# Optimization experiments

Hardware: AMD Instinct MI355X
Metric: run time of the kernel (lower is better)

## Reference

```python
import jax, jax.numpy as jnp
import numpy as np

N_NODES = 100000
IN_CH = 65
HID_CH = 64
N_EDGES = 3200000


def setup_inputs() -> dict:
    key = jax.random.key(0)
    k1, k2, k3, k4, k5 = jax.random.split(key, 5)
    x = jax.random.normal(k1, (N_NODES, IN_CH), dtype=jnp.float32)
    edge_index = jax.random.randint(k2, (2, N_EDGES), 0, N_NODES, dtype=jnp.int64)
    edge_weight = jax.random.uniform(k3, (N_EDGES,), dtype=jnp.float32)
    # PyG GraphConv params: lin_rel (with bias) applied to aggregated neighbors,
    # lin_root (no bias) applied to self features.
    scale = 1.0 / np.sqrt(IN_CH)
    W_rel = jax.random.uniform(k4, (HID_CH, IN_CH), dtype=jnp.float32, minval=-scale, maxval=scale)
    b_rel = jnp.zeros((HID_CH,), dtype=jnp.float32)
    W_root = jax.random.uniform(k5, (HID_CH, IN_CH), dtype=jnp.float32, minval=-scale, maxval=scale)
    return {"x": x, "edge_index": edge_index, "edge_weight": edge_weight,
            "W_rel": W_rel, "b_rel": b_rel, "W_root": W_root}


def reference(x, edge_index, edge_weight, W_rel, b_rel, W_root):
    src = edge_index[0]  # source nodes (x_j in PyG message)
    dst = edge_index[1]  # target nodes (aggregation index)
    # gather neighbor features, weight by edge weight: [E, IN_CH]
    msgs = x[src] * edge_weight[:, None]
    # scatter-add to destination nodes: [N, IN_CH]
    aggr = jax.ops.segment_sum(msgs, dst, num_segments=N_NODES)
    # out = lin_rel(aggr) + lin_root(x)
    out = aggr @ W_rel.T + b_rel + x @ W_root.T
    return out
```

## Files before the change

### kernel.cpp

```cpp
#include <hip/hip_runtime.h>

#define IN_CH 65
#define HID 64
#define BN 64
#define NB 1563
#define CAP 2560
#define SCAP 2432
#define EPB 16384
#define TPS 1024
#define EPT (EPB / TPS)
#define WSTR 132

static inline size_t align16(size_t v) { return (v + 15) & ~(size_t)15; }

__device__ inline ushort f2bf(float f) {
    uint u = __float_as_uint(f);
    return (ushort)((u + 0x7FFF + ((u >> 16) & 1)) >> 16);
}

__global__ __launch_bounds__(256) void k1y(const float* __restrict__ x,
                                           const float* __restrict__ W_rel,
                                           ushort* __restrict__ y16,
                                           int* __restrict__ cnt, int nBuckets,
                                           int nNodes) {
    __shared__ float xsT[65 * 132];
    __shared__ float ws[65 * 68];
    const int tid = threadIdx.x;
    const int tx = tid & 7;
    const int ty = tid >> 3;
    const long nodeBase = (long)blockIdx.x * 128;
    const int nValid = (int)min((long)128, (long)nNodes - nodeBase);

    if (cnt) {
        const int c2 = blockIdx.x * 2;
        if (tid == 0 && c2 < nBuckets) cnt[c2] = 0;
        if (tid == 1 && c2 + 1 < nBuckets) cnt[c2 + 1] = 0;
    }

    for (int f = tid; f < HID * IN_CH; f += 256) {
        const int j = f / IN_CH, c = f - j * IN_CH;
        ws[c * 68 + j] = W_rel[f];
    }
    const float* xsrc = x + nodeBase * IN_CH;
    for (int f = tid; f < 128 * IN_CH; f += 256) {
        const int node = f / IN_CH, k = f - node * IN_CH;
        xsT[k * 132 + node] = (node < nValid) ? xsrc[f] : 0.f;
    }
    __syncthreads();

    float acc[4][8];
#pragma unroll
    for (int i = 0; i < 4; ++i)
#pragma unroll
        for (int j = 0; j < 8; ++j) acc[i][j] = 0.f;

    const int r0 = ty * 4;
    const int c0 = tx * 8;
    for (int k = 0; k < IN_CH; ++k) {
        const float4 a4 = *(const float4*)&xsT[k * 132 + r0];
        const float4 b0 = *(const float4*)&ws[k * 68 + c0];
        const float4 b1 = *(const float4*)&ws[k * 68 + c0 + 4];
        const float aa[4] = {a4.x, a4.y, a4.z, a4.w};
        const float bb[8] = {b0.x, b0.y, b0.z, b0.w, b1.x, b1.y, b1.z, b1.w};
#pragma unroll
        for (int i = 0; i < 4; ++i)
#pragma unroll
            for (int j = 0; j < 8; ++j) acc[i][j] += aa[i] * bb[j];
    }

#pragma unroll
    for (int i = 0; i < 4; ++i) {
        const long node = nodeBase + r0 + i;
        if (node >= nNodes) break;
        uint4 pk;
        pk.x = (uint)f2bf(acc[i][0]) | ((uint)f2bf(acc[i][1]) << 16);
        pk.y = (uint)f2bf(acc[i][2]) | ((uint)f2bf(acc[i][3]) << 16);
        pk.z = (uint)f2bf(acc[i][4]) | ((uint)f2bf(acc[i][5]) << 16);
        pk.w = (uint)f2bf(acc[i][6]) | ((uint)f2bf(acc[i][7]) << 16);
        *(uint4*)&y16[node * HID + c0] = pk;
    }
}

__global__ __launch_bounds__(TPS) void scatterB(const int* __restrict__ ei,
                                                const float* __restrict__ ew,
                                                int* __restrict__ cnt,
                                                int2* __restrict__ pairs, int E) {
    __shared__ int lhist[NB];
    __shared__ int lbase[NB];
    const int tid = threadIdx.x;
    const long e0 = (long)blockIdx.x * EPB;
    const int n = (int)min((long)EPB, (long)E - e0);

    for (int i = tid; i < NB; i += TPS) lhist[i] = 0;
    __syncthreads();

    int dstv[EPT], srcv[EPT];
    float wv[EPT];
#pragma unroll
    for (int k = 0; k < EPT; ++k) {
        const int i = tid + k * TPS;
        const bool valid = i < n;
        dstv[k] = valid ? ei[(long)E + e0 + i] : 0;
        srcv[k] = valid ? ei[e0 + i] : 0;
        wv[k]   = valid ? ew[e0 + i] : 0.f;
        if (valid) atomicAdd(&lhist[dstv[k] >> 6], 1);
    }
    __syncthreads();

    for (int i = tid; i < NB; i += TPS) {
        const int c = lhist[i];
        lbase[i] = c ? atomicAdd(&cnt[i], c) : 0;
        lhist[i] = 0;
    }
    __syncthreads();

#pragma unroll
    for (int k = 0; k < EPT; ++k) {
        const int i = tid + k * TPS;
        if (i < n) {
            const int b = dstv[k] >> 6;
            const int p = lbase[b] + atomicAdd(&lhist[b], 1);
            if (p < CAP)
                pairs[(size_t)b * CAP + p] =
                    make_int2((srcv[k] << 7) | ((dstv[k] & (BN - 1)) << 25),
                              __float_as_int(wv[k]));
        }
    }
}

__global__ __launch_bounds__(512) void aggregateS16(const int2* __restrict__ pairs,
                                                    const int* __restrict__ cnt,
                                                    const ushort* __restrict__ y16,
                                                    const float* __restrict__ x,
                                                    const float* __restrict__ W_root,
                                                    const float* __restrict__ b_rel,
                                                    float* __restrict__ out, int N) {
    __shared__ __align__(16) char smem[19456 + 17408 + 4 * (BN + BN + 1 + BN) + 16];
    float* xs       = (float*)smem;
    int2*  sorted   = (int2*)smem;
    float* rootBuf  = (float*)(smem + 19456);
    int*   sH       = (int*)(smem + 36864);
    int*   soff     = sH + BN;
    int*   scur     = soff + BN + 1;

    const int tid = threadIdx.x;
    const int lane = tid & 63;
    const int wvid = tid >> 6;
    const int half = lane >> 5;
    const uint lane4 = (lane & 31) * 4;
    const int b = blockIdx.x;
    const long nodeBase = (long)b * BN;

    const int m = min(cnt[b], CAP);
    const int2* pb = pairs + (size_t)b * CAP;

    int2 pv[5];
#pragma unroll
    for (int kk = 0; kk < 5; ++kk) {
        const int i = tid + kk * 512;
        if (i < m) pv[kk] = pb[i];
    }

    const int nValid = (int)min((long)BN, (long)N - nodeBase);
    const int nx = nValid * IN_CH;
    const float* xsrc = x + nodeBase * IN_CH;
    for (int i = tid; i < BN * IN_CH; i += 512) xs[i] = (i < nx) ? xsrc[i] : 0.f;

    if (tid < BN) { sH[tid] = 0; scur[tid] = 0; }
    __syncthreads();

#pragma unroll
    for (int kk = 0; kk < 5; ++kk) {
        const int i = tid + kk * 512;
        if (i < m) atomicAdd(&sH[(uint)pv[kk].x >> 25], 1);
    }

    {
        const int wvu = __builtin_amdgcn_readfirstlane(wvid);
        const int c0 = wvu * 8;
        float racc[8];
#pragma unroll
        for (int j = 0; j < 8; ++j) racc[j] = b_rel[c0 + j];
        const float* xrow = xs + lane * IN_CH;
        const float* wb = W_root + (size_t)c0 * IN_CH;
        for (int k = 0; k < IN_CH; ++k) {
            const float xv = xrow[k];
#pragma unroll
            for (int j = 0; j < 8; ++j) racc[j] += xv * wb[j * IN_CH + k];
        }
        float* rb = rootBuf + lane * 68 + c0;
        *(float4*)(rb + 0) = make_float4(racc[0], racc[1], racc[2], racc[3]);
        *(float4*)(rb + 4) = make_float4(racc[4], racc[5], racc[6], racc[7]);
    }
    __syncthreads();

    for (int off = 1; off < BN; off <<= 1) {
        int v = 0;
        if (tid < BN) {
            v = sH[tid];
            if (tid >= off) v += sH[tid - off];
        }
        __syncthreads();
        if (tid < BN) sH[tid] = v;
        __syncthreads();
    }
    if (tid < BN) soff[tid + 1] = sH[tid];
    if (tid == 0) soff[0] = 0;
    __syncthreads();

#pragma unroll
    for (int kk = 0; kk < 5; ++kk) {
        const int i = tid + kk * 512;
        if (i < m) {
            const int d = (uint)pv[kk].x >> 25;
            const int slot = soff[d] + atomicAdd(&scur[d], 1);
            if (slot < SCAP) sorted[slot] = make_int2(pv[kk].x & 0x00FFFF80, pv[kk].y);
        }
    }
    __syncthreads();

    const char* yb = (const char*)y16;
    for (int nl = wvid; nl < BN; nl += 8) {
        const long node = nodeBase + nl;
        if (node >= N) break;
        const int kbeg = min(soff[nl], SCAP);
        const int kend = min(soff[nl + 1], SCAP);
        float ax = 0.f, ay = 0.f;
        int k = kbeg + half;
        for (; k + 14 < kend; k += 16) {
            int2 pp[8];
#pragma unroll
            for (int j = 0; j < 8; ++j) pp[j] = sorted[k + 2 * j];
            uint qq[8];
#pragma unroll
            for (int j = 0; j < 8; ++j)
                qq[j] = *(const uint*)(yb + (uint)pp[j].x + lane4);
#pragma unroll
            for (int j = 0; j < 8; ++j) {
                const float w = __int_as_float(pp[j].y);
                ax += w * __uint_as_float(qq[j] << 16);
                ay += w * __uint_as_float(qq[j] & 0xFFFF0000u);
            }
        }
        for (; k + 6 < kend; k += 8) {
            const int2 p0 = sorted[k],     p1 = sorted[k + 2];
            const int2 p2 = sorted[k + 4], p3 = sorted[k + 6];
            const uint q0 = *(const uint*)(yb + (uint)p0.x + lane4);
            const uint q1 = *(const uint*)(yb + (uint)p1.x + lane4);
            const uint q2 = *(const uint*)(yb + (uint)p2.x + lane4);
            const uint q3 = *(const uint*)(yb + (uint)p3.x + lane4);
            const float w0 = __int_as_float(p0.y), w1 = __int_as_float(p1.y);
            const float w2 = __int_as_float(p2.y), w3 = __int_as_float(p3.y);
            ax += w0 * __uint_as_float(q0 << 16);
            ay += w0 * __uint_as_float(q0 & 0xFFFF0000u);
            ax += w1 * __uint_as_float(q1 << 16);
            ay += w1 * __uint_as_float(q1 & 0xFFFF0000u);
            ax += w2 * __uint_as_float(q2 << 16);
            ay += w2 * __uint_as_float(q2 & 0xFFFF0000u);
            ax += w3 * __uint_as_float(q3 << 16);
            ay += w3 * __uint_as_float(q3 & 0xFFFF0000u);
        }
        for (; k < kend; k += 2) {
            const int2 p = sorted[k];
            const uint q = *(const uint*)(yb + (uint)p.x + lane4);
            const float w = __int_as_float(p.y);
            ax += w * __uint_as_float(q << 16);
            ay += w * __uint_as_float(q & 0xFFFF0000u);
        }
        ax += __shfl_xor(ax, 32);
        ay += __shfl_xor(ay, 32);
        if (half == 0) {
            const float2 rb = *(const float2*)&rootBuf[nl * 68 + (lane & 31) * 2];
            float2* o = (float2*)(out + node * HID) + (lane & 31);
            *o = make_float2(rb.x + ax, rb.y + ay);
        }
    }
}

__global__ __launch_bounds__(256) void k1_full(const float* __restrict__ x,
                                               const float* __restrict__ W_rel,
                                               const float* __restrict__ b_rel,
                                               const float* __restrict__ W_root,
                                               ushort* __restrict__ y16,
                                               float* __restrict__ out,
                                               int nNodes) {
    __shared__ float xs[64 * IN_CH];
    __shared__ float ws[IN_CH * WSTR];
    const int tid = threadIdx.x;
    const int tx = tid & 15;
    const int ty = tid >> 4;
    const long nodeBase = (long)blockIdx.x * 64;
    const int nValid = min(64, nNodes - (int)nodeBase);
    const int nx = nValid * IN_CH;

    for (int f = tid; f < HID * IN_CH; f += 256) {
        const int j = f / IN_CH, c = f - j * IN_CH;
        ws[c * WSTR + j] = W_rel[f];
    }
    for (int f = tid; f < HID * IN_CH; f += 256) {
        const int j = f / IN_CH, c = f - j * IN_CH;
        ws[c * WSTR + HID + j] = W_root[f];
    }
    const float* xsrc = x + nodeBase * IN_CH;
    for (int i = tid; i < 64 * IN_CH; i += 256) xs[i] = (i < nx) ? xsrc[i] : 0.f;
    __syncthreads();

    float acc[4][8];
#pragma unroll
    for (int i = 0; i < 4; ++i)
#pragma unroll
        for (int j = 0; j < 8; ++j) acc[i][j] = 0.f;

    const int r0 = ty * 4;
    const int c0 = tx * 8;
    for (int k = 0; k < IN_CH; ++k) {
        float aa[4] = {xs[(r0 + 0) * IN_CH + k], xs[(r0 + 1) * IN_CH + k],
                       xs[(r0 + 2) * IN_CH + k], xs[(r0 + 3) * IN_CH + k]};
        float4 b0 = *(const float4*)&ws[k * WSTR + c0];
        float4 b1 = *(const float4*)&ws[k * WSTR + c0 + 4];
        float bb[8] = {b0.x, b0.y, b0.z, b0.w, b1.x, b1.y, b1.z, b1.w};
#pragma unroll
        for (int i = 0; i < 4; ++i)
#pragma unroll
            for (int j = 0; j < 8; ++j) acc[i][j] += aa[i] * bb[j];
    }

    if (c0 >= HID) {
        const int h0 = c0 - HID;
        float4 bb0 = *(const float4*)&b_rel[h0];
        float4 bb1 = *(const float4*)&b_rel[h0 + 4];
        float bv[8] = {bb0.x, bb0.y, bb0.z, bb0.w, bb1.x, bb1.y, bb1.z, bb1.w};
#pragma unroll
        for (int i = 0; i < 4; ++i)
#pragma unroll
            for (int j = 0; j < 8; ++j) acc[i][j] += bv[j];
    }

#pragma unroll
    for (int i = 0; i < 4; ++i) {
        const long node = nodeBase + r0 + i;
        if (node >= nNodes) break;
        if (c0 < HID) {
            uint4 pk;
            pk.x = (uint)f2bf(acc[i][0]) | ((uint)f2bf(acc[i][1]) << 16);
            pk.y = (uint)f2bf(acc[i][2]) | ((uint)f2bf(acc[i][3]) << 16);
            pk.z = (uint)f2bf(acc[i][4]) | ((uint)f2bf(acc[i][5]) << 16);
            pk.w = (uint)f2bf(acc[i][6]) | ((uint)f2bf(acc[i][7]) << 16);
            *(uint4*)&y16[node * HID + c0] = pk;
        } else {
            float* dst = out + node * HID + (c0 - HID);
            *(float4*)(dst + 0) = make_float4(acc[i][0], acc[i][1], acc[i][2], acc[i][3]);
            *(float4*)(dst + 4) = make_float4(acc[i][4], acc[i][5], acc[i][6], acc[i][7]);
        }
    }
}

__global__ __launch_bounds__(256) void k2_atomic16(const int* __restrict__ ei,
                                                   const float* __restrict__ ew,
                                                   const ushort* __restrict__ y16,
                                                   float* __restrict__ out, int E) {
    const long t = (long)blockIdx.x * 256 + threadIdx.x;
    const long e = t >> 4;
    const int r = (int)(t & 15);
    if (e >= E) return;
    const int src = ei[e];
    const int dst = ei[(long)E + e];
    const float w = ew[e];
    const uint2 q = ((const uint2*)y16)[(size_t)src * 16 + r];
    float* o = out + (size_t)dst * HID + r * 4;
    unsafeAtomicAdd(o + 0, w * __uint_as_float(q.x << 16));
    unsafeAtomicAdd(o + 1, w * __uint_as_float(q.x & 0xFFFF0000u));
    unsafeAtomicAdd(o + 2, w * __uint_as_float(q.y << 16));
    unsafeAtomicAdd(o + 3, w * __uint_as_float(q.y & 0xFFFF0000u));
}

extern "C" void kernel_launch(void* const* d_in, const int* in_sizes, int n_in,
                              void* d_out, int out_size, void* d_ws, size_t ws_size,
                              hipStream_t stream) {
    const float* x      = (const float*)d_in[0];
    const int*   ei     = (const int*)d_in[1];
    const float* ew     = (const float*)d_in[2];
    const float* W_rel  = (const float*)d_in[3];
    const float* b_rel  = (const float*)d_in[4];
    const float* W_root = (const float*)d_in[5];
    float* out = (float*)d_out;

    const int N = in_sizes[0] / IN_CH;
    const int E = in_sizes[2];

    char* base = (char*)d_ws;
    const size_t oY     = 0;
    const size_t oPairs = align16((size_t)N * HID * 2);
    const size_t oCnt   = oPairs + align16((size_t)NB * CAP * 8);
    const size_t need   = oCnt + (size_t)NB * 4;

    ushort* y16 = (ushort*)(base + oY);
    const int nb1 = (N + 127) / 128;

    const bool fits = (ws_size >= need) && (N <= (1 << 17)) &&
                      ((size_t)NB * BN >= (size_t)N) && ((long)E <= (long)N * 33) &&
                      (2 * nb1 >= NB);

    if (fits) {
        int2* pairs = (int2*)(base + oPairs);
        int*  cnt   = (int*)(base + oCnt);

        k1y<<<nb1, 256, 0, stream>>>(x, W_rel, y16, cnt, NB, N);
        scatterB<<<(E + EPB - 1) / EPB, TPS, 0, stream>>>(ei, ew, cnt, pairs, E);
        aggregateS16<<<NB, 512, 0, stream>>>(pairs, cnt, y16, x, W_root, b_rel, out, N);
    } else {
        const int nbf = (N + 63) / 64;
        k1_full<<<nbf, 256, 0, stream>>>(x, W_rel, b_rel, W_root, y16, out, N);
        const long thr2 = (long)E * 16;
        k2_atomic16<<<(int)((thr2 + 255) / 256), 256, 0, stream>>>(ei, ew, y16, out, E);
    }
}
```

Measured before the change: 234.9 us.

## Move root linear projection into first GEMM kernel, store partial output

The x·W_root^T + b_rel term is now computed in the first kernel alongside the W_rel projection, sharing the x tile in LDS, and written straight to out. The aggregate kernel no longer loads x or runs the per-block root matmul. It reads the partial output back and adds the neighbour sum, which cuts its LDS footprint and serial work. The cost is an extra fp32 write and read of the output plus doubled accumulator registers in the first kernel.

```diff
diff --git a/kernel.cpp b/kernel.cpp
--- a/kernel.cpp
+++ b/kernel.cpp
@@ -18,13 +18,16 @@
     return (ushort)((u + 0x7FFF + ((u >> 16) & 1)) >> 16);
 }
 
-__global__ __launch_bounds__(256) void k1y(const float* __restrict__ x,
-                                           const float* __restrict__ W_rel,
-                                           ushort* __restrict__ y16,
-                                           int* __restrict__ cnt, int nBuckets,
-                                           int nNodes) {
+__global__ __launch_bounds__(256) void k1both(const float* __restrict__ x,
+                                              const float* __restrict__ W_rel,
+                                              const float* __restrict__ W_root,
+                                              const float* __restrict__ b_rel,
+                                              ushort* __restrict__ y16,
+                                              float* __restrict__ out,
+                                              int* __restrict__ cnt, int nBuckets,
+                                              int nNodes) {
     __shared__ float xsT[65 * 132];
-    __shared__ float ws[65 * 68];
+    __shared__ float ws[65 * 136];
     const int tid = threadIdx.x;
     const int tx = tid & 7;
     const int ty = tid >> 3;
@@ -39,7 +42,11 @@
 
     for (int f = tid; f < HID * IN_CH; f += 256) {
         const int j = f / IN_CH, c = f - j * IN_CH;
-        ws[c * 68 + j] = W_rel[f];
+        ws[c * 136 + j] = W_rel[f];
+    }
+    for (int f = tid; f < HID * IN_CH; f += 256) {
+        const int j = f / IN_CH, c = f - j * IN_CH;
+        ws[c * 136 + 68 + j] = W_root[f];
     }
     const float* xsrc = x + nodeBase * IN_CH;
     for (int f = tid; f < 128 * IN_CH; f += 256) {
@@ -48,24 +55,40 @@
     }
     __syncthreads();
 
-    float acc[4][8];
+    float accY[4][8], accR[4][8];
 #pragma unroll
     for (int i = 0; i < 4; ++i)
 #pragma unroll
-        for (int j = 0; j < 8; ++j) acc[i][j] = 0.f;
+        for (int j = 0; j < 8; ++j) { accY[i][j] = 0.f; accR[i][j] = 0.f; }
 
     const int r0 = ty * 4;
     const int c0 = tx * 8;
     for (int k = 0; k < IN_CH; ++k) {
         const float4 a4 = *(const float4*)&xsT[k * 132 + r0];
-        const float4 b0 = *(const float4*)&ws[k * 68 + c0];
-        const float4 b1 = *(const float4*)&ws[k * 68 + c0 + 4];
+        const float4 y0 = *(const float4*)&ws[k * 136 + c0];
+        const float4 y1 = *(const float4*)&ws[k * 136 + c0 + 4];
+        const float4 q0 = *(const float4*)&ws[k * 136 + 68 + c0];
+        const float4 q1 = *(const float4*)&ws[k * 136 + 68 + c0 + 4];
         const float aa[4] = {a4.x, a4.y, a4.z, a4.w};
-        const float bb[8] = {b0.x, b0.y, b0.z, b0.w, b1.x, b1.y, b1.z, b1.w};
+        const float by[8] = {y0.x, y0.y, y0.z, y0.w, y1.x, y1.y, y1.z, y1.w};
+        const float br[8] = {q0.x, q0.y, q0.z, q0.w, q1.x, q1.y, q1.z, q1.w};
 #pragma unroll
         for (int i = 0; i < 4; ++i)
 #pragma unroll
-            for (int j = 0; j < 8; ++j) acc[i][j] += aa[i] * bb[j];
+            for (int j = 0; j < 8; ++j) {
+                accY[i][j] += aa[i] * by[j];
+                accR[i][j] += aa[i] * br[j];
+            }
+    }
+
+    {
+        const float4 bb0 = *(const float4*)&b_rel[c0];
+        const float4 bb1 = *(const float4*)&b_rel[c0 + 4];
+        const float bv[8] = {bb0.x, bb0.y, bb0.z, bb0.w, bb1.x, bb1.y, bb1.z, bb1.w};
+#pragma unroll
+        for (int i = 0; i < 4; ++i)
+#pragma unroll
+            for (int j = 0; j < 8; ++j) accR[i][j] += bv[j];
     }
 
 #pragma unroll
@@ -73,11 +96,14 @@
         const long node = nodeBase + r0 + i;
         if (node >= nNodes) break;
         uint4 pk;
-        pk.x = (uint)f2bf(acc[i][0]) | ((uint)f2bf(acc[i][1]) << 16);
-        pk.y = (uint)f2bf(acc[i][2]) | ((uint)f2bf(acc[i][3]) << 16);
-        pk.z = (uint)f2bf(acc[i][4]) | ((uint)f2bf(acc[i][5]) << 16);
-        pk.w = (uint)f2bf(acc[i][6]) | ((uint)f2bf(acc[i][7]) << 16);
+        pk.x = (uint)f2bf(accY[i][0]) | ((uint)f2bf(accY[i][1]) << 16);
+        pk.y = (uint)f2bf(accY[i][2]) | ((uint)f2bf(accY[i][3]) << 16);
+        pk.z = (uint)f2bf(accY[i][4]) | ((uint)f2bf(accY[i][5]) << 16);
+        pk.w = (uint)f2bf(accY[i][6]) | ((uint)f2bf(accY[i][7]) << 16);
         *(uint4*)&y16[node * HID + c0] = pk;
+        float* dst = out + node * HID + c0;
+        *(float4*)(dst + 0) = make_float4(accR[i][0], accR[i][1], accR[i][2], accR[i][3]);
+        *(float4*)(dst + 4) = make_float4(accR[i][4], accR[i][5], accR[i][6], accR[i][7]);
     }
 }
 
@@ -131,25 +157,19 @@
 __global__ __launch_bounds__(512) void aggregateS16(const int2* __restrict__ pairs,
                                                     const int* __restrict__ cnt,
                                                     const ushort* __restrict__ y16,
-                                                    const float* __restrict__ x,
-                                                    const float* __restrict__ W_root,
-                                                    const float* __restrict__ b_rel,
                                                     float* __restrict__ out, int N) {
-    __shared__ __align__(16) char smem[19456 + 17408 + 4 * (BN + BN + 1 + BN) + 16];
-    float* xs       = (float*)smem;
-    int2*  sorted   = (int2*)smem;
-    float* rootBuf  = (float*)(smem + 19456);
-    int*   sH       = (int*)(smem + 36864);
-    int*   soff     = sH + BN;
-    int*   scur     = soff + BN + 1;
-
+    __shared__ int2 sorted[SCAP];
+    __shared__ int sH[BN];
+    __shared__ int soff[BN + 1];
+    __shared__ int scur[BN];
     const int tid = threadIdx.x;
     const int lane = tid & 63;
     const int wvid = tid >> 6;
     const int half = lane >> 5;
     const uint lane4 = (lane & 31) * 4;
     const int b = blockIdx.x;
-    const long nodeBase = (long)b * BN;
+
+    if (tid < BN) { sH[tid] = 0; scur[tid] = 0; }
 
     const int m = min(cnt[b], CAP);
     const int2* pb = pairs + (size_t)b * CAP;
@@ -160,37 +180,12 @@
         const int i = tid + kk * 512;
         if (i < m) pv[kk] = pb[i];
     }
-
-    const int nValid = (int)min((long)BN, (long)N - nodeBase);
-    const int nx = nValid * IN_CH;
-    const float* xsrc = x + nodeBase * IN_CH;
-    for (int i = tid; i < BN * IN_CH; i += 512) xs[i] = (i < nx) ? xsrc[i] : 0.f;
-
-    if (tid < BN) { sH[tid] = 0; scur[tid] = 0; }
     __syncthreads();
 
 #pragma unroll
     for (int kk = 0; kk < 5; ++kk) {
         const int i = tid + kk * 512;
         if (i < m) atomicAdd(&sH[(uint)pv[kk].x >> 25], 1);
-    }
-
-    {
-        const int wvu = __builtin_amdgcn_readfirstlane(wvid);
-        const int c0 = wvu * 8;
-        float racc[8];
-#pragma unroll
-        for (int j = 0; j < 8; ++j) racc[j] = b_rel[c0 + j];
-        const float* xrow = xs + lane * IN_CH;
-        const float* wb = W_root + (size_t)c0 * IN_CH;
-        for (int k = 0; k < IN_CH; ++k) {
-            const float xv = xrow[k];
-#pragma unroll
-            for (int j = 0; j < 8; ++j) racc[j] += xv * wb[j * IN_CH + k];
-        }
-        float* rb = rootBuf + lane * 68 + c0;
-        *(float4*)(rb + 0) = make_float4(racc[0], racc[1], racc[2], racc[3]);
-        *(float4*)(rb + 4) = make_float4(racc[4], racc[5], racc[6], racc[7]);
     }
     __syncthreads();
 
@@ -220,11 +215,14 @@
     __syncthreads();
 
     const char* yb = (const char*)y16;
+    const long nodeBase = (long)b * BN;
     for (int nl = wvid; nl < BN; nl += 8) {
         const long node = nodeBase + nl;
         if (node >= N) break;
         const int kbeg = min(soff[nl], SCAP);
         const int kend = min(soff[nl + 1], SCAP);
+        float2* o = (float2*)(out + node * HID) + (lane & 31);
+        const float2 cur = *o;
         float ax = 0.f, ay = 0.f;
         int k = kbeg + half;
         for (; k + 14 < kend; k += 16) {
@@ -270,9 +268,7 @@
         ax += __shfl_xor(ax, 32);
         ay += __shfl_xor(ay, 32);
         if (half == 0) {
-            const float2 rb = *(const float2*)&rootBuf[nl * 68 + (lane & 31) * 2];
-            float2* o = (float2*)(out + node * HID) + (lane & 31);
-            *o = make_float2(rb.x + ax, rb.y + ay);
+            *o = make_float2(cur.x + ax, cur.y + ay);
         }
     }
 }
@@ -405,9 +401,9 @@
         int2* pairs = (int2*)(base + oPairs);
         int*  cnt   = (int*)(base + oCnt);
 
-        k1y<<<nb1, 256, 0, stream>>>(x, W_rel, y16, cnt, NB, N);
+        k1both<<<nb1, 256, 0, stream>>>(x, W_rel, W_root, b_rel, y16, out, cnt, NB, N);
         scatterB<<<(E + EPB - 1) / EPB, TPS, 0, stream>>>(ei, ew, cnt, pairs, E);
-        aggregateS16<<<NB, 512, 0, stream>>>(pairs, cnt, y16, x, W_root, b_rel, out, N);
+        aggregateS16<<<NB, 512, 0, stream>>>(pairs, cnt, y16, out, N);
     } else {
         const int nbf = (N + 63) / 64;
         k1_full<<<nbf, 256, 0, stream>>>(x, W_rel, b_rel, W_root, y16, out, N);
```

New measurement: 247.3 us. +5.3%, slower.
